# Kernel optimization log

Measured on AMD Instinct MI355X. Metric: run time of the kernel, lower is better.

The kernel has to match this reference:

```python
import jax, jax.numpy as jnp
import numpy as np

B, C, H, W = 32, 512, 32, 32
N_WORDS, WORD_DIM = 77, 256
HW2 = H * W


def setup_inputs() -> dict:
    key = jax.random.key(0)
    k1, k2, k3 = jax.random.split(key, 3)
    feat = jax.random.normal(k1, (B, C, H, W), dtype=jnp.float32)
    word_emb = jax.random.normal(k2, (B, N_WORDS, WORD_DIM), dtype=jnp.float32)
    # nn.Linear(word_dim, img_hw*img_hw): weight (out,in), bias (out,)
    W_fc = jax.random.normal(k3, (HW2, WORD_DIM), dtype=jnp.float32) * (1.0 / np.sqrt(WORD_DIM))
    b_fc = jnp.zeros((HW2,), dtype=jnp.float32)
    return {"feat": feat, "word_emb": word_emb, "W_fc": W_fc, "b_fc": b_fc}


def reference(feat, word_emb, W_fc, b_fc):
    b, c, h, w = feat.shape
    f = feat.reshape(b, c, h * w)                                   # (b, c, hw2)
    we = jnp.einsum('bnd,kd->bnk', word_emb, W_fc) + b_fc           # (b, n, hw2)
    we = jnp.swapaxes(we, 1, 2)                                     # (b, hw2, n)
    scores = jnp.einsum('bck,bkn->bcn', f, we)                      # (b, c, n)
    att = jax.nn.softmax(scores, axis=-1)                           # (b, c, n)
    att_feat = jnp.einsum('bcn,bkn->bck', att, we)                  # (b, c, hw2)
    return att_feat.reshape(b, c, h, w)
```

## Files before the change

### kernel.cpp

```cpp
#include <hip/hip_runtime.h>

#define B_    32
#define C_    512
#define HW2_  1024
#define NW    77
#define NP    80
#define NPT   96
#define WD    256

typedef unsigned int   uint32;
typedef unsigned short u16;
typedef __attribute__((ext_vector_type(8))) short bf16x8;
typedef __attribute__((ext_vector_type(4))) float f32x4;

#define MFMA(a, b, c) __builtin_amdgcn_mfma_f32_16x16x32_bf16(a, b, c, 0, 0, 0)

__device__ __forceinline__ void split1(float x, u16 &h, u16 &l) {
    uint32 u = __float_as_uint(x);
    h = (u16)(u >> 16);
    float r = x - __uint_as_float(u & 0xffff0000u);
    uint32 v = __float_as_uint(r);
    l = (u16)((v + 0x7fffu + ((v >> 16) & 1u)) >> 16);
}

__device__ __forceinline__ void split8(float4 a, float4 b, bf16x8 &h, bf16x8 &l) {
    float v[8] = {a.x, a.y, a.z, a.w, b.x, b.y, b.z, b.w};
    #pragma unroll
    for (int i = 0; i < 8; ++i) {
        u16 hh, ll; split1(v[i], hh, ll);
        h[i] = (short)hh; l[i] = (short)ll;
    }
}

__global__ __launch_bounds__(256) void we_gemm(
    const float* __restrict__ word_emb, const float* __restrict__ W_fc,
    const float* __restrict__ b_fc,
    bf16x8* __restrict__ we_hi, bf16x8* __restrict__ we_lo,
    bf16x8* __restrict__ weT_hi, bf16x8* __restrict__ weT_lo)
{
    __shared__ __align__(16) float D[NP][68];

    const int id   = blockIdx.x;
    const int b    = id >> 4;
    const int kb   = (id & 15) * 64;
    const int t    = threadIdx.x;
    const int w    = t >> 6, lane = t & 63;
    const int lr   = lane & 15, lg = lane >> 4;
    const int kout = kb + 16 * w + lr;

    f32x4 acc[5];
    #pragma unroll
    for (int m = 0; m < 5; ++m) acc[m] = (f32x4)0.0f;

    const float* wrow = W_fc + kout * WD;
    const float* emb  = word_emb + b * NW * WD;

    for (int ks = 0; ks < 8; ++ks) {
        const int dk = ks * 32 + 8 * lg;
        bf16x8 bh, bl;
        {   float4 x = *(const float4*)(wrow + dk);
            float4 y = *(const float4*)(wrow + dk + 4);
            split8(x, y, bh, bl); }
        bf16x8 ah[5], al[5];
        #pragma unroll
        for (int m = 0; m < 5; ++m) {
            const int n = 16 * m + lr;
            float4 x = make_float4(0.f, 0.f, 0.f, 0.f), y = x;
            if (n < NW) {
                const float* ap = emb + n * WD + dk;
                x = *(const float4*)ap; y = *(const float4*)(ap + 4);
            }
            split8(x, y, ah[m], al[m]);
        }
        #pragma unroll
        for (int m = 0; m < 5; ++m) {
            acc[m] = MFMA(ah[m], bh, acc[m]);
            acc[m] = MFMA(ah[m], bl, acc[m]);
            acc[m] = MFMA(al[m], bh, acc[m]);
            acc[m] = MFMA(al[m], bl, acc[m]);
        }
    }

    const float bias = b_fc[kout];
    #pragma unroll
    for (int m = 0; m < 5; ++m)
        #pragma unroll
        for (int r = 0; r < 4; ++r)
            D[16 * m + 4 * lg + r][16 * w + lr] = acc[m][r] + bias;
    __syncthreads();

    for (int u = t; u < NP * 8; u += 256) {
        const int n = u >> 3, c8 = (u & 7) * 8;
        bf16x8 h, l;
        if (n < NW) {
            float4 x = *(const float4*)&D[n][c8];
            float4 y = *(const float4*)&D[n][c8 + 4];
            split8(x, y, h, l);
        } else { h = (bf16x8)(short)0; l = (bf16x8)(short)0; }
        const int o = ((b * NP + n) * HW2_ + kb + c8) >> 3;
        we_hi[o] = h; we_lo[o] = l;
    }
    if (t < 128) {
        const int kr  = t & 63;
        const int sel = t >> 6;
        bf16x8* dst = (sel ? weT_lo : weT_hi) + (((b * HW2_ + kb + kr) * NPT) >> 3);
        #pragma unroll
        for (int g = 0; g < 12; ++g) {
            bf16x8 v;
            #pragma unroll
            for (int i = 0; i < 8; ++i) {
                const int n = g * 8 + i;
                float x = (n < NW) ? D[n][kr] : 0.f;
                u16 h, l; split1(x, h, l);
                v[i] = (short)(sel ? l : h);
            }
            dst[g] = v;
        }
    }
}

__global__ __launch_bounds__(256, 2) void attn_mfma(
    const float* __restrict__ feat,
    const bf16x8* __restrict__ we_hi, const bf16x8* __restrict__ we_lo,
    const bf16x8* __restrict__ weT_hi, const bf16x8* __restrict__ weT_lo,
    float* __restrict__ out)
{
    __shared__ __align__(16) float S[3][16][84];
    __shared__ __align__(16) u16   Ph[16][NPT];
    __shared__ __align__(16) u16   Pl[16][NPT];

    const int id  = blockIdx.x;
    const int q   = id >> 3;
    const int b   = (id & 7) + 8 * (q >> 5);
    const int c0  = (q & 31) * 16;

    const int t    = threadIdx.x;
    const int h    = t >> 6;
    const int lane = t & 63, lr = lane & 15, lg = lane >> 4;

    f32x4 acc[5];
    #pragma unroll
    for (int m = 0; m < 5; ++m) acc[m] = (f32x4)0.0f;

    const float*  frow = feat + (size_t)(b * C_ + c0 + lr) * HW2_;
    const bf16x8* wh   = we_hi + ((size_t)b * NP * HW2_ >> 3);
    const bf16x8* wl   = we_lo + ((size_t)b * NP * HW2_ >> 3);

    for (int ks = 0; ks < 8; ++ks) {
        const int kk = h * 256 + ks * 32 + 8 * lg;
        bf16x8 fh, fl;
        {   float4 x = *(const float4*)(frow + kk);
            float4 y = *(const float4*)(frow + kk + 4);
            split8(x, y, fh, fl); }
        bf16x8 ah[5], al[5];
        #pragma unroll
        for (int m = 0; m < 5; ++m) {
            const int o = ((16 * m + lr) * HW2_ + kk) >> 3;
            ah[m] = wh[o];
            al[m] = wl[o];
        }
        #pragma unroll
        for (int m = 0; m < 5; ++m) {
            acc[m] = MFMA(ah[m], fh, acc[m]);
            acc[m] = MFMA(ah[m], fl, acc[m]);
            acc[m] = MFMA(al[m], fh, acc[m]);
        }
    }

    if (h < 3) {
        #pragma unroll
        for (int m = 0; m < 5; ++m)
            #pragma unroll
            for (int r = 0; r < 4; ++r)
                S[h][lr][16 * m + 4 * lg + r] = acc[m][r];
    }
    __syncthreads();

    if (h == 3) {
        float sc[5][4], mx = -3.0e38f;
        #pragma unroll
        for (int m = 0; m < 5; ++m)
            #pragma unroll
            for (int r = 0; r < 4; ++r) {
                const int n = 16 * m + 4 * lg + r;
                float v = acc[m][r] + S[0][lr][n] + S[1][lr][n] + S[2][lr][n];
                sc[m][r] = v;
                if (n < NW) mx = fmaxf(mx, v);
            }
        mx = fmaxf(mx, __shfl_xor(mx, 16));
        mx = fmaxf(mx, __shfl_xor(mx, 32));
        float sum = 0.f, e[5][4];
        #pragma unroll
        for (int m = 0; m < 5; ++m)
            #pragma unroll
            for (int r = 0; r < 4; ++r) {
                const int n = 16 * m + 4 * lg + r;
                float v = (n < NW) ? __expf(sc[m][r] - mx) : 0.f;
                e[m][r] = v; sum += v;
            }
        sum += __shfl_xor(sum, 16);
        sum += __shfl_xor(sum, 32);
        const float inv = 1.0f / sum;
        #pragma unroll
        for (int m = 0; m < 5; ++m)
            #pragma unroll
            for (int r = 0; r < 4; ++r) {
                const int n = 16 * m + 4 * lg + r;
                u16 ph, pl; split1(e[m][r] * inv, ph, pl);
                Ph[lr][n] = ph; Pl[lr][n] = pl;
            }
    } else if (h == 0) {
        #pragma unroll
        for (int r = 0; r < 4; ++r) { Ph[lr][80 + 4 * lg + r] = 0; Pl[lr][80 + 4 * lg + r] = 0; }
    }
    __syncthreads();

    bf16x8 pbh[3], pbl[3];
    #pragma unroll
    for (int ksn = 0; ksn < 3; ++ksn) {
        pbh[ksn] = *(const bf16x8*)&Ph[lr][32 * ksn + 8 * lg];
        pbl[ksn] = *(const bf16x8*)&Pl[lr][32 * ksn + 8 * lg];
    }
    const bf16x8* th = weT_hi + ((size_t)b * HW2_ * NPT >> 3);
    const bf16x8* tl = weT_lo + ((size_t)b * HW2_ * NPT >> 3);
    float* orow = out + (size_t)(b * C_ + c0 + lr) * HW2_;

    for (int ci = 0; ci < 4; ++ci) {
        const int kb = (ci * 4 + h) * 64;
        f32x4 o[4];
        #pragma unroll
        for (int kt = 0; kt < 4; ++kt) o[kt] = (f32x4)0.0f;
        #pragma unroll
        for (int kt = 0; kt < 4; ++kt) {
            const int rbase = ((kb + 16 * kt + lr) * NPT) >> 3;
            #pragma unroll
            for (int ksn = 0; ksn < 3; ++ksn) {
                bf16x8 wa = th[rbase + (32 * ksn + 8 * lg) / 8];
                bf16x8 wb = tl[rbase + (32 * ksn + 8 * lg) / 8];
                o[kt] = MFMA(wa, pbh[ksn], o[kt]);
                o[kt] = MFMA(wa, pbl[ksn], o[kt]);
                o[kt] = MFMA(wb, pbh[ksn], o[kt]);
            }
        }
        #pragma unroll
        for (int kt = 0; kt < 4; ++kt) {
            float4 v = make_float4(o[kt][0], o[kt][1], o[kt][2], o[kt][3]);
            *(float4*)(orow + kb + 16 * kt + 4 * lg) = v;
        }
    }
}

extern "C" void kernel_launch(void* const* d_in, const int* in_sizes, int n_in,
                              void* d_out, int out_size, void* d_ws, size_t ws_size,
                              hipStream_t stream) {
    (void)in_sizes; (void)n_in; (void)out_size; (void)ws_size;
    const float* feat     = (const float*)d_in[0];
    const float* word_emb = (const float*)d_in[1];
    const float* W_fc     = (const float*)d_in[2];
    const float* b_fc     = (const float*)d_in[3];

    bf16x8* we_hi  = (bf16x8*)d_ws;
    bf16x8* we_lo  = we_hi  + ((size_t)B_ * NP * HW2_ >> 3);
    bf16x8* weT_hi = we_lo  + ((size_t)B_ * NP * HW2_ >> 3);
    bf16x8* weT_lo = weT_hi + ((size_t)B_ * HW2_ * NPT >> 3);

    we_gemm<<<512, 256, 0, stream>>>(word_emb, W_fc, b_fc, we_hi, we_lo, weT_hi, weT_lo);
    attn_mfma<<<1024, 256, 0, stream>>>(feat, we_hi, we_lo, weT_hi, weT_lo, (float*)d_out);
}
```

Measured before the change: 208.5 us.

## Pre-split inputs to bf16, software-pipeline loads, and spread softmax across warps

Result: slower. 212.9 us (+2.1%).

```diff
diff --git a/kernel.cpp b/kernel.cpp
--- a/kernel.cpp
+++ b/kernel.cpp
@@ -15,6 +15,11 @@
 
 #define MFMA(a, b, c) __builtin_amdgcn_mfma_f32_16x16x32_bf16(a, b, c, 0, 0, 0)
 
+#define WE_ELN   ((size_t)B_ * NP * HW2_ / 8)
+#define WET_ELN  ((size_t)B_ * HW2_ * NPT / 8)
+#define W_ELN    ((size_t)HW2_ * WD / 8)
+#define E_ELN    ((size_t)B_ * NP * WD / 8)
+
 __device__ __forceinline__ void split1(float x, u16 &h, u16 &l) {
     uint32 u = __float_as_uint(x);
     h = (u16)(u >> 16);
@@ -32,77 +37,101 @@
     }
 }
 
-__global__ __launch_bounds__(256) void we_gemm(
-    const float* __restrict__ word_emb, const float* __restrict__ W_fc,
+__global__ __launch_bounds__(256) void split_pre(
+    const float* __restrict__ W_fc, const float* __restrict__ word_emb,
+    bf16x8* __restrict__ Wh, bf16x8* __restrict__ Wl,
+    bf16x8* __restrict__ Eh, bf16x8* __restrict__ El)
+{
+    const int g = blockIdx.x * 256 + threadIdx.x;
+    if (g < (int)W_ELN) {
+        float4 x = *(const float4*)(W_fc + g * 8);
+        float4 y = *(const float4*)(W_fc + g * 8 + 4);
+        bf16x8 h, l; split8(x, y, h, l);
+        Wh[g] = h; Wl[g] = l;
+    } else {
+        const int e = g - (int)W_ELN;
+        const int b = e / 2560, r = e % 2560;
+        const int n = r >> 5, gg = r & 31;
+        bf16x8 h = (bf16x8)(short)0, l = h;
+        if (n < NW) {
+            const float* p = word_emb + ((size_t)(b * NW + n)) * WD + gg * 8;
+            float4 x = *(const float4*)p, y = *(const float4*)(p + 4);
+            split8(x, y, h, l);
+        }
+        Eh[e] = h; El[e] = l;
+    }
+}
+
+__global__ __launch_bounds__(256, 2) void we_gemm(
+    const bf16x8* __restrict__ Wh, const bf16x8* __restrict__ Wl,
+    const bf16x8* __restrict__ Eh, const bf16x8* __restrict__ El,
     const float* __restrict__ b_fc,
     bf16x8* __restrict__ we_hi, bf16x8* __restrict__ we_lo,
     bf16x8* __restrict__ weT_hi, bf16x8* __restrict__ weT_lo)
 {
-    __shared__ __align__(16) float D[NP][68];
-
-    const int id   = blockIdx.x;
-    const int b    = id >> 4;
-    const int kb   = (id & 15) * 64;
-    const int t    = threadIdx.x;
-    const int w    = t >> 6, lane = t & 63;
-    const int lr   = lane & 15, lg = lane >> 4;
+    __shared__ __align__(16) uint32 HL[NP][68];
+
+    const int id = blockIdx.x;
+    const int b  = (id & 7) + 8 * (id >> 7);
+    const int kb = ((id >> 3) & 15) * 64;
+    const int t  = threadIdx.x;
+    const int w  = t >> 6, lane = t & 63, lr = lane & 15, lg = lane >> 4;
     const int kout = kb + 16 * w + lr;
 
     f32x4 acc[5];
     #pragma unroll
     for (int m = 0; m < 5; ++m) acc[m] = (f32x4)0.0f;
 
-    const float* wrow = W_fc + kout * WD;
-    const float* emb  = word_emb + b * NW * WD;
-
+    const bf16x8* wrh = Wh + kout * 32;
+    const bf16x8* wrl = Wl + kout * 32;
+    const bf16x8* ebh = Eh + (b * NP + lr) * 32;
+    const bf16x8* ebl = El + (b * NP + lr) * 32;
+
+    #pragma unroll
     for (int ks = 0; ks < 8; ++ks) {
-        const int dk = ks * 32 + 8 * lg;
-        bf16x8 bh, bl;
-        {   float4 x = *(const float4*)(wrow + dk);
-            float4 y = *(const float4*)(wrow + dk + 4);
-            split8(x, y, bh, bl); }
-        bf16x8 ah[5], al[5];
+        const int o = ks * 4 + lg;
+        const bf16x8 bh = wrh[o], bl = wrl[o];
         #pragma unroll
         for (int m = 0; m < 5; ++m) {
-            const int n = 16 * m + lr;
-            float4 x = make_float4(0.f, 0.f, 0.f, 0.f), y = x;
-            if (n < NW) {
-                const float* ap = emb + n * WD + dk;
-                x = *(const float4*)ap; y = *(const float4*)(ap + 4);
+            const bf16x8 ah = ebh[m * 512 + o];
+            const bf16x8 al = ebl[m * 512 + o];
+            acc[m] = MFMA(ah, bh, acc[m]);
+            acc[m] = MFMA(ah, bl, acc[m]);
+            acc[m] = MFMA(al, bh, acc[m]);
+            acc[m] = MFMA(al, bl, acc[m]);
+        }
+    }
+
+    const float bias = b_fc[kout];
+    #pragma unroll
+    for (int m = 0; m < 5; ++m)
+        #pragma unroll
+        for (int r = 0; r < 4; ++r) {
+            u16 hh, ll; split1(acc[m][r] + bias, hh, ll);
+            HL[16 * m + 4 * lg + r][16 * w + lr] = ((uint32)hh << 16) | ll;
+        }
+    __syncthreads();
+
+    #pragma unroll
+    for (int u0 = 0; u0 < 640; u0 += 256) {
+        const int u = u0 + t;
+        if (u < 640) {
+            const int n = u >> 3, c8 = (u & 7) * 8;
+            uint4 p0 = *(const uint4*)&HL[n][c8];
+            uint4 p1 = *(const uint4*)&HL[n][c8 + 4];
+            const uint32 pw[8] = {p0.x, p0.y, p0.z, p0.w, p1.x, p1.y, p1.z, p1.w};
+            bf16x8 hv, lv;
+            #pragma unroll
+            for (int i = 0; i < 8; ++i) {
+                hv[i] = (short)(pw[i] >> 16);
+                lv[i] = (short)(pw[i] & 0xffffu);
             }
-            split8(x, y, ah[m], al[m]);
-        }
-        #pragma unroll
-        for (int m = 0; m < 5; ++m) {
-            acc[m] = MFMA(ah[m], bh, acc[m]);
-            acc[m] = MFMA(ah[m], bl, acc[m]);
-            acc[m] = MFMA(al[m], bh, acc[m]);
-            acc[m] = MFMA(al[m], bl, acc[m]);
-        }
-    }
-
-    const float bias = b_fc[kout];
-    #pragma unroll
-    for (int m = 0; m < 5; ++m)
-        #pragma unroll
-        for (int r = 0; r < 4; ++r)
-            D[16 * m + 4 * lg + r][16 * w + lr] = acc[m][r] + bias;
-    __syncthreads();
-
-    for (int u = t; u < NP * 8; u += 256) {
-        const int n = u >> 3, c8 = (u & 7) * 8;
-        bf16x8 h, l;
-        if (n < NW) {
-            float4 x = *(const float4*)&D[n][c8];
-            float4 y = *(const float4*)&D[n][c8 + 4];
-            split8(x, y, h, l);
-        } else { h = (bf16x8)(short)0; l = (bf16x8)(short)0; }
-        const int o = ((b * NP + n) * HW2_ + kb + c8) >> 3;
-        we_hi[o] = h; we_lo[o] = l;
+            const int o = ((b * NP + n) * HW2_ + kb + c8) >> 3;
+            we_hi[o] = hv; we_lo[o] = lv;
+        }
     }
     if (t < 128) {
-        const int kr  = t & 63;
-        const int sel = t >> 6;
+        const int kr = t & 63, sel = t >> 6;
         bf16x8* dst = (sel ? weT_lo : weT_hi) + (((b * HW2_ + kb + kr) * NPT) >> 3);
         #pragma unroll
         for (int g = 0; g < 12; ++g) {
@@ -110,29 +139,27 @@
             #pragma unroll
             for (int i = 0; i < 8; ++i) {
                 const int n = g * 8 + i;
-                float x = (n < NW) ? D[n][kr] : 0.f;
-                u16 h, l; split1(x, h, l);
-                v[i] = (short)(sel ? l : h);
+                const uint32 p = (n < NP) ? HL[n][kr] : 0u;
+                v[i] = (short)(sel ? (p & 0xffffu) : (p >> 16));
             }
             dst[g] = v;
         }
     }
 }
 
-__global__ __launch_bounds__(256, 2) void attn_mfma(
+__global__ __launch_bounds__(256, 3) void attn_mfma(
     const float* __restrict__ feat,
     const bf16x8* __restrict__ we_hi, const bf16x8* __restrict__ we_lo,
     const bf16x8* __restrict__ weT_hi, const bf16x8* __restrict__ weT_lo,
     float* __restrict__ out)
 {
-    __shared__ __align__(16) float S[3][16][84];
+    __shared__ __align__(16) float S[4][16][84];
     __shared__ __align__(16) u16   Ph[16][NPT];
     __shared__ __align__(16) u16   Pl[16][NPT];
 
     const int id  = blockIdx.x;
-    const int q   = id >> 3;
-    const int b   = (id & 7) + 8 * (q >> 5);
-    const int c0  = (q & 31) * 16;
+    const int b   = (id & 7) + 8 * (id >> 8);
+    const int c0  = ((id >> 3) & 31) * 16;
 
     const int t    = threadIdx.x;
     const int h    = t >> 6;
@@ -143,75 +170,84 @@
     for (int m = 0; m < 5; ++m) acc[m] = (f32x4)0.0f;
 
     const float*  frow = feat + (size_t)(b * C_ + c0 + lr) * HW2_;
-    const bf16x8* wh   = we_hi + ((size_t)b * NP * HW2_ >> 3);
-    const bf16x8* wl   = we_lo + ((size_t)b * NP * HW2_ >> 3);
-
+    const bf16x8* wh   = we_hi + (size_t)b * (NP * HW2_ / 8);
+    const bf16x8* wl   = we_lo + (size_t)b * (NP * HW2_ / 8);
+
+    float4 fx[2], fy[2];
+    bf16x8 AH[2][5], AL[2][5];
+
+#define P1_LOAD(slot, ksv) do {                                   \
+        const int kk_ = h * 256 + (ksv) * 32 + 8 * lg;            \
+        fx[slot] = *(const float4*)(frow + kk_);                  \
+        fy[slot] = *(const float4*)(frow + kk_ + 4);              \
+        const int go_ = h * 32 + (ksv) * 4 + lg;                  \
+        _Pragma("unroll")                                         \
+        for (int m_ = 0; m_ < 5; ++m_) {                          \
+            AH[slot][m_] = wh[(16 * m_ + lr) * 128 + go_];        \
+            AL[slot][m_] = wl[(16 * m_ + lr) * 128 + go_];        \
+        } } while (0)
+
+    P1_LOAD(0, 0);
+    #pragma unroll
     for (int ks = 0; ks < 8; ++ks) {
-        const int kk = h * 256 + ks * 32 + 8 * lg;
-        bf16x8 fh, fl;
-        {   float4 x = *(const float4*)(frow + kk);
-            float4 y = *(const float4*)(frow + kk + 4);
-            split8(x, y, fh, fl); }
-        bf16x8 ah[5], al[5];
+        if (ks < 7) {
+            if ((ks & 1) == 0) P1_LOAD(1, ks + 1);
+            else               P1_LOAD(0, ks + 1);
+        }
+        const int cur = ks & 1;
+        bf16x8 fh, fl; split8(fx[cur], fy[cur], fh, fl);
         #pragma unroll
         for (int m = 0; m < 5; ++m) {
-            const int o = ((16 * m + lr) * HW2_ + kk) >> 3;
-            ah[m] = wh[o];
-            al[m] = wl[o];
-        }
-        #pragma unroll
-        for (int m = 0; m < 5; ++m) {
-            acc[m] = MFMA(ah[m], fh, acc[m]);
-            acc[m] = MFMA(ah[m], fl, acc[m]);
-            acc[m] = MFMA(al[m], fh, acc[m]);
-        }
-    }
-
-    if (h < 3) {
-        #pragma unroll
-        for (int m = 0; m < 5; ++m)
-            #pragma unroll
-            for (int r = 0; r < 4; ++r)
-                S[h][lr][16 * m + 4 * lg + r] = acc[m][r];
-    }
+            acc[m] = MFMA(AH[cur][m], fh, acc[m]);
+            acc[m] = MFMA(AH[cur][m], fl, acc[m]);
+            acc[m] = MFMA(AL[cur][m], fh, acc[m]);
+        }
+    }
+#undef P1_LOAD
+
+    #pragma unroll
+    for (int m = 0; m < 5; ++m)
+        #pragma unroll
+        for (int r = 0; r < 4; ++r)
+            S[h][lr][16 * m + 4 * lg + r] = acc[m][r];
     __syncthreads();
 
-    if (h == 3) {
-        float sc[5][4], mx = -3.0e38f;
-        #pragma unroll
-        for (int m = 0; m < 5; ++m)
-            #pragma unroll
-            for (int r = 0; r < 4; ++r) {
-                const int n = 16 * m + 4 * lg + r;
-                float v = acc[m][r] + S[0][lr][n] + S[1][lr][n] + S[2][lr][n];
-                sc[m][r] = v;
-                if (n < NW) mx = fmaxf(mx, v);
+    {
+        const int srow = 4 * h + (lane >> 4), scol = lane & 15;
+        float v5[6];
+        float mx = -3.0e38f;
+        #pragma unroll
+        for (int j = 0; j < 6; ++j) {
+            const int n = scol + 16 * j;
+            float sv = 0.f;
+            if (j < 5) {
+                sv = S[0][srow][n] + S[1][srow][n] + S[2][srow][n] + S[3][srow][n];
+                if (n < NW) mx = fmaxf(mx, sv);
             }
-        mx = fmaxf(mx, __shfl_xor(mx, 16));
-        mx = fmaxf(mx, __shfl_xor(mx, 32));
-        float sum = 0.f, e[5][4];
-        #pragma unroll
-        for (int m = 0; m < 5; ++m)
-            #pragma unroll
-            for (int r = 0; r < 4; ++r) {
-                const int n = 16 * m + 4 * lg + r;
-                float v = (n < NW) ? __expf(sc[m][r] - mx) : 0.f;
-                e[m][r] = v; sum += v;
-            }
-        sum += __shfl_xor(sum, 16);
-        sum += __shfl_xor(sum, 32);
+            v5[j] = sv;
+        }
+        mx = fmaxf(mx, __shfl_xor(mx, 1));
+        mx = fmaxf(mx, __shfl_xor(mx, 2));
+        mx = fmaxf(mx, __shfl_xor(mx, 4));
+        mx = fmaxf(mx, __shfl_xor(mx, 8));
+        float sum = 0.f;
+        #pragma unroll
+        for (int j = 0; j < 6; ++j) {
+            const int n = scol + 16 * j;
+            const float e = (n < NW) ? __expf(v5[j] - mx) : 0.f;
+            v5[j] = e; sum += e;
+        }
+        sum += __shfl_xor(sum, 1);
+        sum += __shfl_xor(sum, 2);
+        sum += __shfl_xor(sum, 4);
+        sum += __shfl_xor(sum, 8);
         const float inv = 1.0f / sum;
         #pragma unroll
-        for (int m = 0; m < 5; ++m)
-            #pragma unroll
-            for (int r = 0; r < 4; ++r) {
-                const int n = 16 * m + 4 * lg + r;
-                u16 ph, pl; split1(e[m][r] * inv, ph, pl);
-                Ph[lr][n] = ph; Pl[lr][n] = pl;
-            }
-    } else if (h == 0) {
-        #pragma unroll
-        for (int r = 0; r < 4; ++r) { Ph[lr][80 + 4 * lg + r] = 0; Pl[lr][80 + 4 * lg + r] = 0; }
+        for (int j = 0; j < 6; ++j) {
+            const int n = scol + 16 * j;
+            u16 ph, pl; split1(v5[j] * inv, ph, pl);
+            Ph[srow][n] = ph; Pl[srow][n] = pl;
+        }
     }
     __syncthreads();
 
@@ -221,33 +257,48 @@
         pbh[ksn] = *(const bf16x8*)&Ph[lr][32 * ksn + 8 * lg];
         pbl[ksn] = *(const bf16x8*)&Pl[lr][32 * ksn + 8 * lg];
     }
-    const bf16x8* th = weT_hi + ((size_t)b * HW2_ * NPT >> 3);
-    const bf16x8* tl = weT_lo + ((size_t)b * HW2_ * NPT >> 3);
+    const bf16x8* th = weT_hi + (size_t)b * (HW2_ * NPT / 8);
+    const bf16x8* tl = weT_lo + (size_t)b * (HW2_ * NPT / 8);
     float* orow = out + (size_t)(b * C_ + c0 + lr) * HW2_;
 
+    bf16x8 WA[3], WB[3];
+
+#define P3_LOAD(slot, g) do {                                     \
+        const int ci_ = (g) / 12, s_ = (g) % 12;                  \
+        const int kt_ = s_ & 3, ksn_ = s_ >> 2;                   \
+        const int row_ = (ci_ * 4 + h) * 64 + 16 * kt_ + lr;      \
+        const int off_ = row_ * 12 + 4 * ksn_ + lg;               \
+        WA[slot] = th[off_]; WB[slot] = tl[off_]; } while (0)
+
+    P3_LOAD(0, 0);
+    P3_LOAD(1, 1);
+    #pragma unroll
     for (int ci = 0; ci < 4; ++ci) {
-        const int kb = (ci * 4 + h) * 64;
         f32x4 o[4];
         #pragma unroll
         for (int kt = 0; kt < 4; ++kt) o[kt] = (f32x4)0.0f;
         #pragma unroll
-        for (int kt = 0; kt < 4; ++kt) {
-            const int rbase = ((kb + 16 * kt + lr) * NPT) >> 3;
-            #pragma unroll
-            for (int ksn = 0; ksn < 3; ++ksn) {
-                bf16x8 wa = th[rbase + (32 * ksn + 8 * lg) / 8];
-                bf16x8 wb = tl[rbase + (32 * ksn + 8 * lg) / 8];
-                o[kt] = MFMA(wa, pbh[ksn], o[kt]);
-                o[kt] = MFMA(wa, pbl[ksn], o[kt]);
-                o[kt] = MFMA(wb, pbh[ksn], o[kt]);
+        for (int s = 0; s < 12; ++s) {
+            const int g = ci * 12 + s;
+            if (g < 46) {
+                const int sl = (g + 2) % 3;
+                if (sl == 0)      P3_LOAD(0, g + 2);
+                else if (sl == 1) P3_LOAD(1, g + 2);
+                else              P3_LOAD(2, g + 2);
             }
-        }
+            const int cs = g % 3, kt = s & 3, ksn = s >> 2;
+            o[kt] = MFMA(WA[cs], pbh[ksn], o[kt]);
+            o[kt] = MFMA(WA[cs], pbl[ksn], o[kt]);
+            o[kt] = MFMA(WB[cs], pbh[ksn], o[kt]);
+        }
+        const int kb2 = (ci * 4 + h) * 64;
         #pragma unroll
         for (int kt = 0; kt < 4; ++kt) {
             float4 v = make_float4(o[kt][0], o[kt][1], o[kt][2], o[kt][3]);
-            *(float4*)(orow + kb + 16 * kt + 4 * lg) = v;
-        }
-    }
+            *(float4*)(orow + kb2 + 16 * kt + 4 * lg) = v;
+        }
+    }
+#undef P3_LOAD
 }
 
 extern "C" void kernel_launch(void* const* d_in, const int* in_sizes, int n_in,
@@ -260,10 +311,15 @@
     const float* b_fc     = (const float*)d_in[3];
 
     bf16x8* we_hi  = (bf16x8*)d_ws;
-    bf16x8* we_lo  = we_hi  + ((size_t)B_ * NP * HW2_ >> 3);
-    bf16x8* weT_hi = we_lo  + ((size_t)B_ * NP * HW2_ >> 3);
-    bf16x8* weT_lo = weT_hi + ((size_t)B_ * HW2_ * NPT >> 3);
-
-    we_gemm<<<512, 256, 0, stream>>>(word_emb, W_fc, b_fc, we_hi, we_lo, weT_hi, weT_lo);
+    bf16x8* we_lo  = we_hi  + WE_ELN;
+    bf16x8* weT_hi = we_lo  + WE_ELN;
+    bf16x8* weT_lo = weT_hi + WET_ELN;
+    bf16x8* Wh     = weT_lo + WET_ELN;
+    bf16x8* Wl     = Wh + W_ELN;
+    bf16x8* Eh     = Wl + W_ELN;
+    bf16x8* El     = Eh + E_ELN;
+
+    split_pre<<<448, 256, 0, stream>>>(W_fc, word_emb, Wh, Wl, Eh, El);
+    we_gemm<<<512, 256, 0, stream>>>(Wh, Wl, Eh, El, b_fc, we_hi, we_lo, weT_hi, weT_lo);
     attn_mfma<<<1024, 256, 0, stream>>>(feat, we_hi, we_lo, weT_hi, weT_lo, (float*)d_out);
 }
```
